# Kernel optimization log

Measured on AMD Instinct MI355X. Metric: run time of the kernel, lower is better.

Reference implementation:

```python
import jax, jax.numpy as jnp
import numpy as np
from jax import lax

T = 16        # in_length
E = 32        # input_embedding_size_d
H = 64        # encoder_size
NG = 32       # vehicles per scene group
G = 1024      # number of scene groups
N = G * NG    # total vehicles
C = 3         # class_num

leaky = lambda x: jax.nn.leaky_relu(x, 0.1)

def _gru_final(x_seq, Wih, Whh, bih, bhh):
    # x_seq: (T, N, E). PyTorch GRU gate order: r, z, n. Returns final hidden (N, H).
    def step(h, x):
        gx = x @ Wih.T + bih
        gh = h @ Whh.T + bhh
        xr, xz, xn = jnp.split(gx, 3, axis=-1)
        hr, hz, hn = jnp.split(gh, 3, axis=-1)
        r = jax.nn.sigmoid(xr + hr)
        z = jax.nn.sigmoid(xz + hz)
        ng = jnp.tanh(xn + r * hn)
        return (1.0 - z) * ng + z * h, None
    h0 = jnp.zeros((x_seq.shape[1], Whh.shape[1]), x_seq.dtype)
    hT, _ = lax.scan(step, h0, x_seq)
    return hT

def setup_inputs() -> dict:
    key = jax.random.key(0)
    ks = jax.random.split(key, 24)
    def rn(k, shape, fan):
        return jax.random.normal(k, shape, jnp.float32) * np.float32(1.0 / np.sqrt(fan))
    inp = {}
    inp["scene"] = jax.random.normal(ks[0], (N, 2 * T), jnp.float32)
    inp["condition"] = jax.random.randint(ks[1], (N,), 0, C, jnp.int32)
    inp["hero_pos_index"] = jax.random.randint(ks[2], (G,), 0, N, jnp.int32)
    inp["nbrs_pos_index"] = jax.random.randint(ks[3], (N,), 0, N, jnp.int32)
    inp["index_div"] = jnp.arange(N, dtype=jnp.int32).reshape(G, NG)
    # ip_emb_d: Linear(2, E)
    inp["W_emb"] = rn(ks[4], (2, E), 2)
    inp["b_emb"] = jnp.zeros((E,), jnp.float32)
    # forward / backward GRUs (weight_ih: (3H,E), weight_hh: (3H,H))
    inp["Wih_f"] = rn(ks[5], (3 * H, E), E); inp["Whh_f"] = rn(ks[6], (3 * H, H), H)
    inp["bih_f"] = jnp.zeros((3 * H,), jnp.float32); inp["bhh_f"] = jnp.zeros((3 * H,), jnp.float32)
    inp["Wih_b"] = rn(ks[7], (3 * H, E), E); inp["Whh_b"] = rn(ks[8], (3 * H, H), H)
    inp["bih_b"] = jnp.zeros((3 * H,), jnp.float32); inp["bhh_b"] = jnp.zeros((3 * H,), jnp.float32)
    # mlp: Linear(H, H//2)
    inp["Wm"] = rn(ks[9], (H, H // 2), H); inp["bm"] = jnp.zeros((H // 2,), jnp.float32)
    # spatial_mlp: Linear(2T, H) -> Linear(H, H//2)
    inp["Ws1"] = rn(ks[10], (2 * T, H), 2 * T); inp["bs1"] = jnp.zeros((H,), jnp.float32)
    inp["Ws2"] = rn(ks[11], (H, H // 2), H); inp["bs2"] = jnp.zeros((H // 2,), jnp.float32)
    # op_d: Linear(H, H//4) -> Linear(H//4, C)
    inp["Wo1"] = rn(ks[12], (H, H // 4), H); inp["bo1"] = jnp.zeros((H // 4,), jnp.float32)
    inp["Wo2"] = rn(ks[13], (H // 4, C), H // 4); inp["bo2"] = jnp.zeros((C,), jnp.float32)
    return inp

def reference(scene, condition, hero_pos_index, nbrs_pos_index, index_div,
              W_emb, b_emb, Wih_f, Whh_f, bih_f, bhh_f, Wih_b, Whh_b, bih_b, bhh_b,
              Wm, bm, Ws1, bs1, Ws2, bs2, Wo1, bo1, Wo2, bo2):
    n_total = scene.shape[0]
    # scene.view(-1,2,T).permute(2,0,1) -> (T, N, 2)
    scene_t = scene.reshape(n_total, 2, T).transpose(2, 0, 1)
    emb = leaky(scene_t @ W_emb + b_emb)                 # (T, N, E)
    h_f = _gru_final(emb, Wih_f, Whh_f, bih_f, bhh_f)    # (N, H)
    h_b = _gru_final(emb[::-1], Wih_b, Whh_b, bih_b, bhh_b)
    seq_enc = leaky(((h_f + h_b) * 0.5) @ Wm + bm)       # (N, H//2)
    # pairwise relative features within each group: rel[g, j, i] = x_i - x_j
    feat_g = scene[index_div]                            # (G, n, 2T); row layout == permute(1,2,0).view(-1,2T)
    rel = feat_g[:, None, :, :] - feat_g[:, :, None, :]  # (G, n, n, 2T)
    enc = leaky(leaky(rel @ Ws1 + bs1) @ Ws2 + bs2)      # (G, n, n, H//2)
    # diagonal pairs (i==j) are dropped in the original; subtract mlp(0) then divide by n-1
    zero_enc = leaky(leaky(bs1) @ Ws2 + bs2)             # (H//2,)
    n_grp = index_div.shape[1]
    pooled = (enc.sum(axis=2) - zero_enc) / (n_grp - 1)  # (G, n, H//2)
    pooled = pooled.reshape(n_total, -1)                 # group-concat order == vehicle order (arange groups)
    full_enc = jnp.concatenate([seq_enc, pooled], axis=1)  # (N, H)
    x_logit = leaky(full_enc @ Wo1 + bo1) @ Wo2 + bo2      # (N, C)
    return x_logit, full_enc
```

## Files before the change

### kernel.cpp

```cpp
#include <hip/hip_runtime.h>
#include <hip/hip_bf16.h>

#define TT 16
#define EE 32
#define HH 64
#define NGRP 32
#define CC 3

typedef __attribute__((ext_vector_type(8))) short short8;
typedef __attribute__((ext_vector_type(4))) short short4v;
typedef __attribute__((ext_vector_type(4))) float floatx4;

#define MFMA16(a, b, c) __builtin_amdgcn_mfma_f32_16x16x32_bf16((a), (b), (c), 0, 0, 0)

#define RLN2 1.4426950408889634f

__device__ __forceinline__ float leakyf(float x) { return fmaxf(x, 0.1f * x); }
__device__ __forceinline__ short f2bf(float x) {
    unsigned u = __float_as_uint(x);
    return (short)((u + 0x7FFFu + ((u >> 16) & 1u)) >> 16);
}
__device__ __forceinline__ short f2bf_h(float x) {
    return (short)((__float_as_uint(x) + 0x8000u) >> 16);
}
__device__ __forceinline__ float bf2f(short s) {
    return __uint_as_float(((unsigned)(unsigned short)s) << 16);
}
__device__ __forceinline__ short8 ld8bf(const float* __restrict__ p) {
    const float4 a = *(const float4*)p;
    const float4 b = *(const float4*)(p + 4);
    short8 v;
    v[0] = f2bf(a.x); v[1] = f2bf(a.y); v[2] = f2bf(a.z); v[3] = f2bf(a.w);
    v[4] = f2bf(b.x); v[5] = f2bf(b.y); v[6] = f2bf(b.z); v[7] = f2bf(b.w);
    return v;
}
__device__ __forceinline__ short8 ld8bfs(const float* __restrict__ p, float s) {
    const float4 a = *(const float4*)p;
    const float4 b = *(const float4*)(p + 4);
    short8 v;
    v[0] = f2bf(a.x * s); v[1] = f2bf(a.y * s); v[2] = f2bf(a.z * s); v[3] = f2bf(a.w * s);
    v[4] = f2bf(b.x * s); v[5] = f2bf(b.y * s); v[6] = f2bf(b.z * s); v[7] = f2bf(b.w * s);
    return v;
}

__global__ __launch_bounds__(512, 4) void fused_kernel(
    const float* __restrict__ scene, const int* __restrict__ index_div,
    const float* __restrict__ W_emb, const float* __restrict__ b_emb,
    const float* __restrict__ Wih_f, const float* __restrict__ Whh_f,
    const float* __restrict__ bih_f, const float* __restrict__ bhh_f,
    const float* __restrict__ Wih_b, const float* __restrict__ Whh_b,
    const float* __restrict__ bih_b, const float* __restrict__ bhh_b,
    const float* __restrict__ Wm, const float* __restrict__ bm,
    const float* __restrict__ Ws1, const float* __restrict__ bs1,
    const float* __restrict__ Ws2, const float* __restrict__ bs2,
    const float* __restrict__ Wo1, const float* __restrict__ bo1,
    const float* __restrict__ Wo2, const float* __restrict__ bo2,
    float* __restrict__ full_enc, float* __restrict__ out)
{
    __shared__ float sscene[32][33];
    __shared__ __align__(16) union SmemU {
        struct {
            short Hf[2 * 2 * 2 * 2 * 64 * 8];
            short Xb[2 * 2 * 2 * 64 * 8];
        } g;
        struct {
            short Hf_keep[2 * 2 * 2 * 2 * 64 * 8];
            float su[NGRP][68];
            float fe[NGRP][68];
            float szero[32];
        } s;
    } sm;

    const int g    = blockIdx.x;
    const int tid  = threadIdx.x;
    const int lane = tid & 63;
    const int w    = __builtin_amdgcn_readfirstlane(tid >> 6);
    const int dir  = w >> 2;
    const int wd   = w & 3;
    const int cc   = lane & 15;
    const int quad = lane >> 4;
    const int j    = wd * 16 + cc;
    const int ks_w = j >> 5;
    const int qa_w = (j >> 3) & 3;
    const int ii_w = j & 7;
    const int rlane = (lane & 48) | ((lane & 3) << 2) | ((lane >> 2) & 3);

    #pragma unroll
    for (int rep = 0; rep < 2; ++rep) {
        const int idx = tid + rep * 512;
        const int v = idx >> 5, c = idx & 31;
        const int n = index_div[g * NGRP + v];
        sscene[c][v] = scene[n * 32 + c];
    }

    const float* Wih = dir ? Wih_b : Wih_f;
    const float* Whh = dir ? Whh_b : Whh_f;
    const float* bih = dir ? bih_b : bih_f;
    const float* bhh = dir ? bhh_b : bhh_f;
    const int k0 = quad * 8;
    const float SRZ = -RLN2, SN = 2.0f * RLN2;
    const short8 Br0  = ld8bfs(Whh + (j      ) * 64 + k0,      SRZ);
    const short8 Br1  = ld8bfs(Whh + (j      ) * 64 + 32 + k0, SRZ);
    const short8 Br2  = ld8bfs(Wih + (j      ) * 32 + k0,      SRZ);
    const short8 Bz0  = ld8bfs(Whh + (j +  64) * 64 + k0,      SRZ);
    const short8 Bz1  = ld8bfs(Whh + (j +  64) * 64 + 32 + k0, SRZ);
    const short8 Bz2  = ld8bfs(Wih + (j +  64) * 32 + k0,      SRZ);
    const short8 Bhn0 = ld8bfs(Whh + (j + 128) * 64 + k0,      SN);
    const short8 Bhn1 = ld8bfs(Whh + (j + 128) * 64 + 32 + k0, SN);
    const short8 Bxn  = ld8bfs(Wih + (j + 128) * 32 + k0,      SN);
    const float vb_r  = SRZ * (bih[j] + bhh[j]);
    const float vb_z  = SRZ * (bih[j + 64] + bhh[j + 64]);
    const float vb_xn = SN * bih[j + 128];
    const float vb_hn = SN * bhh[j + 128];

    const int l     = tid & 255;
    const int veh_x = l & 31;
    const int q2    = l >> 5;
    const int e0    = q2 * 4;
    float w0e[4], w1e[4], bbe[4];
    #pragma unroll
    for (int d = 0; d < 4; ++d) {
        w0e[d] = W_emb[e0 + d];
        w1e[d] = W_emb[EE + e0 + d];
        bbe[d] = b_emb[e0 + d];
    }
    const int xoff = dir * 2048 + ((veh_x >> 4) * 64 + (q2 >> 1) * 16 + (veh_x & 15)) * 8
                   + (q2 & 1) * 4;

    __syncthreads();

    {
        const short8 z8 = {0, 0, 0, 0, 0, 0, 0, 0};
        *(short8*)&sm.g.Hf[(tid >> 8) * 4096 + (tid & 255) * 8] = z8;
        const int t0 = dir ? (TT - 1) : 0;
        const float xs = sscene[t0][veh_x];
        const float ys = sscene[16 + t0][veh_x];
        short4v v;
        #pragma unroll
        for (int d = 0; d < 4; ++d)
            v[d] = f2bf_h(leakyf(fmaf(xs, w0e[d], fmaf(ys, w1e[d], bbe[d]))));
        *(short4v*)&sm.g.Xb[xoff] = v;
    }

    float h_reg[8];
    #pragma unroll
    for (int i = 0; i < 8; ++i) h_reg[i] = 0.0f;

    const int hf_dir = dir * 4096;
    __syncthreads();

    #pragma unroll 2
    for (int s = 0; s < TT; ++s) {
        const int pb = s & 1, nb = pb ^ 1;
        const short* HfD = &sm.g.Hf[hf_dir + pb * 2048];
        short*       HfN = &sm.g.Hf[hf_dir + nb * 2048];
        const short* XbD = &sm.g.Xb[dir * 2048 + pb * 1024];
        #pragma unroll
        for (int mt = 0; mt < 2; ++mt) {
            const short8 Ah0 = *(const short8*)&HfD[((0 * 2 + mt) * 64 + rlane) * 8];
            const short8 Ah1 = *(const short8*)&HfD[((1 * 2 + mt) * 64 + rlane) * 8];
            const short8 Axx = *(const short8*)&XbD[(mt * 64 + lane) * 8];
            const floatx4 z4 = {0.f, 0.f, 0.f, 0.f};
            const floatx4 ar  = MFMA16(Axx, Br2, MFMA16(Ah1, Br1, MFMA16(Ah0, Br0, z4)));
            const floatx4 az  = MFMA16(Axx, Bz2, MFMA16(Ah1, Bz1, MFMA16(Ah0, Bz0, z4)));
            const floatx4 ahn = MFMA16(Ah1, Bhn1, MFMA16(Ah0, Bhn0, z4));
            const floatx4 axn = MFMA16(Axx, Bxn, z4);
            #pragma unroll
            for (int r = 0; r < 4; ++r) {
                const float rr = __builtin_amdgcn_rcpf(1.0f + __builtin_amdgcn_exp2f(ar[r] + vb_r));
                const float zz = __builtin_amdgcn_rcpf(1.0f + __builtin_amdgcn_exp2f(az[r] + vb_z));
                const float y  = fmaf(rr, ahn[r] + vb_hn, axn[r] + vb_xn);
                const float ng = fmaf(-2.0f,
                                      __builtin_amdgcn_rcpf(__builtin_amdgcn_exp2f(y) + 1.0f),
                                      1.0f);
                const float h0 = h_reg[mt * 4 + r];
                h_reg[mt * 4 + r] = fmaf(zz, h0 - ng, ng);
            }
        }
        #pragma unroll
        for (int mt = 0; mt < 2; ++mt) {
            #pragma unroll
            for (int r = 0; r < 4; ++r) {
                const int slot = qa_w * 16 + r * 4 + quad;
                HfN[((ks_w * 2 + mt) * 64 + slot) * 8 + ii_w] = f2bf_h(h_reg[mt * 4 + r]);
            }
        }
        if (s + 1 < TT) {
            const int tn = dir ? (TT - 2 - s) : (s + 1);
            const float xs = sscene[tn][veh_x];
            const float ys = sscene[16 + tn][veh_x];
            short4v v;
            #pragma unroll
            for (int d = 0; d < 4; ++d)
                v[d] = f2bf_h(leakyf(fmaf(xs, w0e[d], fmaf(ys, w1e[d], bbe[d]))));
            *(short4v*)&sm.g.Xb[xoff + nb * 1024] = v;
        }
        __syncthreads();
    }

    if (w < 4) {
        const int nt   = w >> 1;
        const int mt_e = w & 1;
        const int n_col = nt * 16 + cc;
        short8 Bm0, Bm1;
        #pragma unroll
        for (int i = 0; i < 8; ++i) {
            Bm0[i] = f2bf(Wm[(     quad * 8 + i) * 32 + n_col]);
            Bm1[i] = f2bf(Wm[(32 + quad * 8 + i) * 32 + n_col]);
        }
        short8 A0, A1;
        #pragma unroll
        for (int ks = 0; ks < 2; ++ks) {
            const short8 F = *(const short8*)&sm.g.Hf[0    + ((ks * 2 + mt_e) * 64 + rlane) * 8];
            const short8 B = *(const short8*)&sm.g.Hf[4096 + ((ks * 2 + mt_e) * 64 + rlane) * 8];
            #pragma unroll
            for (int i = 0; i < 8; ++i) {
                const short v = f2bf(0.5f * (bf2f(F[i]) + bf2f(B[i])));
                if (ks == 0) A0[i] = v; else A1[i] = v;
            }
        }
        const floatx4 z4 = {0.f, 0.f, 0.f, 0.f};
        const floatx4 acc = MFMA16(A1, Bm1, MFMA16(A0, Bm0, z4));
        const float bmn = bm[n_col];
        #pragma unroll
        for (int r = 0; r < 4; ++r) {
            const int veh = mt_e * 16 + quad * 4 + r;
            const float sv = leakyf(acc[r] + bmn);
            const int n = index_div[g * NGRP + veh];
            full_enc[n * HH + n_col] = sv;
            sm.s.fe[veh][n_col] = sv;
        }
    } else {
        const int v  = l >> 3;
        const int d0 = (l & 7) * 8;
        float acc[8];
        #pragma unroll
        for (int i = 0; i < 8; ++i) acc[i] = 0.0f;
        #pragma unroll
        for (int e = 0; e < EE; ++e) {
            const float f = sscene[e][v];
            const float4 w0 = *(const float4*)&Ws1[e * 64 + d0];
            const float4 w1 = *(const float4*)&Ws1[e * 64 + d0 + 4];
            acc[0] = fmaf(f, w0.x, acc[0]); acc[1] = fmaf(f, w0.y, acc[1]);
            acc[2] = fmaf(f, w0.z, acc[2]); acc[3] = fmaf(f, w0.w, acc[3]);
            acc[4] = fmaf(f, w1.x, acc[4]); acc[5] = fmaf(f, w1.y, acc[5]);
            acc[6] = fmaf(f, w1.z, acc[6]); acc[7] = fmaf(f, w1.w, acc[7]);
        }
        #pragma unroll
        for (int i = 0; i < 8; ++i) sm.s.su[v][d0 + i] = acc[i];
        if (l < 32) {
            float zs = bs2[l];
            #pragma unroll
            for (int d = 0; d < HH; ++d) zs = fmaf(leakyf(bs1[d]), Ws2[d * 32 + l], zs);
            sm.s.szero[l] = leakyf(zs);
        }
    }

    short8 Bw00, Bw01, Bw10, Bw11;
    #pragma unroll
    for (int i = 0; i < 8; ++i) {
        Bw00[i] = f2bf(Ws2[(     quad * 8 + i) * 32 + cc]);
        Bw01[i] = f2bf(Ws2[(32 + quad * 8 + i) * 32 + cc]);
        Bw10[i] = f2bf(Ws2[(     quad * 8 + i) * 32 + 16 + cc]);
        Bw11[i] = f2bf(Ws2[(32 + quad * 8 + i) * 32 + 16 + cc]);
    }
    float bsq0[8], bsq1[8];
    #pragma unroll
    for (int i = 0; i < 8; ++i) {
        bsq0[i] = bs1[quad * 8 + i];
        bsq1[i] = bs1[32 + quad * 8 + i];
    }
    const float bs2c0 = bs2[cc], bs2c1 = bs2[16 + cc];
    __syncthreads();

    float* swo1 = (float*)&sscene[0][0];
    *(float2*)&swo1[tid * 2] = *(const float2*)&Wo1[tid * 2];

    #pragma unroll 2
    for (int jj = 0; jj < 4; ++jj) {
        const int jrow = w * 4 + jj;
        float vj0[8], vj1[8];
        #pragma unroll
        for (int i = 0; i < 8; ++i) {
            vj0[i] = sm.s.su[jrow][quad * 8 + i] - bsq0[i];
            vj1[i] = sm.s.su[jrow][32 + quad * 8 + i] - bsq1[i];
        }
        float acc0 = 0.0f, acc1 = 0.0f;
        #pragma unroll
        for (int it = 0; it < 2; ++it) {
            const int irow = it * 16 + cc;
            const float4 p0 = *(const float4*)&sm.s.su[irow][quad * 8];
            const float4 p1 = *(const float4*)&sm.s.su[irow][quad * 8 + 4];
            const float4 p2 = *(const float4*)&sm.s.su[irow][32 + quad * 8];
            const float4 p3 = *(const float4*)&sm.s.su[irow][32 + quad * 8 + 4];
            short8 A0, A1;
            A0[0] = f2bf(leakyf(p0.x - vj0[0])); A0[1] = f2bf(leakyf(p0.y - vj0[1]));
            A0[2] = f2bf(leakyf(p0.z - vj0[2])); A0[3] = f2bf(leakyf(p0.w - vj0[3]));
            A0[4] = f2bf(leakyf(p1.x - vj0[4])); A0[5] = f2bf(leakyf(p1.y - vj0[5]));
            A0[6] = f2bf(leakyf(p1.z - vj0[6])); A0[7] = f2bf(leakyf(p1.w - vj0[7]));
            A1[0] = f2bf(leakyf(p2.x - vj1[0])); A1[1] = f2bf(leakyf(p2.y - vj1[1]));
            A1[2] = f2bf(leakyf(p2.z - vj1[2])); A1[3] = f2bf(leakyf(p2.w - vj1[3]));
            A1[4] = f2bf(leakyf(p3.x - vj1[4])); A1[5] = f2bf(leakyf(p3.y - vj1[5]));
            A1[6] = f2bf(leakyf(p3.z - vj1[6])); A1[7] = f2bf(leakyf(p3.w - vj1[7]));
            const floatx4 z4 = {0.f, 0.f, 0.f, 0.f};
            const floatx4 D0 = MFMA16(A1, Bw01, MFMA16(A0, Bw00, z4));
            const floatx4 D1 = MFMA16(A1, Bw11, MFMA16(A0, Bw10, z4));
            #pragma unroll
            for (int r = 0; r < 4; ++r) {
                acc0 += leakyf(D0[r] + bs2c0);
                acc1 += leakyf(D1[r] + bs2c1);
            }
        }
        acc0 += __shfl_xor(acc0, 16, 64); acc0 += __shfl_xor(acc0, 32, 64);
        acc1 += __shfl_xor(acc1, 16, 64); acc1 += __shfl_xor(acc1, 32, 64);
        const int n = index_div[g * NGRP + jrow];
        if (quad == 0) {
            const float pv = (acc0 - sm.s.szero[cc]) * (1.0f / 31.0f);
            full_enc[n * HH + 32 + cc] = pv;
            sm.s.fe[jrow][32 + cc] = pv;
        } else if (quad == 1) {
            const float pv = (acc1 - sm.s.szero[16 + cc]) * (1.0f / 31.0f);
            full_enc[n * HH + 48 + cc] = pv;
            sm.s.fe[jrow][48 + cc] = pv;
        }
    }
    __syncthreads();

    {
        const int veh = tid >> 4;
        const int p   = tid & 15;
        float a = bo1[p];
        #pragma unroll
        for (int k = 0; k < HH; ++k)
            a = fmaf(sm.s.fe[veh][k], swo1[k * 16 + p], a);
        a = leakyf(a);
        float l0 = a * Wo2[p * 3 + 0];
        float l1 = a * Wo2[p * 3 + 1];
        float l2 = a * Wo2[p * 3 + 2];
        #pragma unroll
        for (int off = 1; off < 16; off <<= 1) {
            l0 += __shfl_xor(l0, off, 64);
            l1 += __shfl_xor(l1, off, 64);
            l2 += __shfl_xor(l2, off, 64);
        }
        if (p == 0) {
            const int n = index_div[g * NGRP + veh];
            out[n * 3 + 0] = l0 + bo2[0];
            out[n * 3 + 1] = l1 + bo2[1];
            out[n * 3 + 2] = l2 + bo2[2];
        }
    }
}

extern "C" void kernel_launch(void* const* d_in, const int* in_sizes, int n_in,
                              void* d_out, int out_size, void* d_ws, size_t ws_size,
                              hipStream_t stream) {
    const float* scene     = (const float*)d_in[0];
    const int*   index_div = (const int*)d_in[4];
    const float* W_emb = (const float*)d_in[5];
    const float* b_emb = (const float*)d_in[6];
    const float* Wih_f = (const float*)d_in[7];
    const float* Whh_f = (const float*)d_in[8];
    const float* bih_f = (const float*)d_in[9];
    const float* bhh_f = (const float*)d_in[10];
    const float* Wih_b = (const float*)d_in[11];
    const float* Whh_b = (const float*)d_in[12];
    const float* bih_b = (const float*)d_in[13];
    const float* bhh_b = (const float*)d_in[14];
    const float* Wm  = (const float*)d_in[15];
    const float* bm  = (const float*)d_in[16];
    const float* Ws1 = (const float*)d_in[17];
    const float* bs1 = (const float*)d_in[18];
    const float* Ws2 = (const float*)d_in[19];
    const float* bs2 = (const float*)d_in[20];
    const float* Wo1 = (const float*)d_in[21];
    const float* bo1 = (const float*)d_in[22];
    const float* Wo2 = (const float*)d_in[23];
    const float* bo2 = (const float*)d_in[24];

    const int N = in_sizes[0] / (2 * TT);
    const int G = in_sizes[4] / NGRP;

    float* out      = (float*)d_out;
    float* full_enc = out + (size_t)N * CC;

    fused_kernel<<<dim3(G), dim3(512), 0, stream>>>(
        scene, index_div, W_emb, b_emb, Wih_f, Whh_f, bih_f, bhh_f,
        Wih_b, Whh_b, bih_b, bhh_b, Wm, bm, Ws1, bs1, Ws2, bs2,
        Wo1, bo1, Wo2, bo2, full_enc, out);
}
```

Before: 195.4 us.

## Split fused kernel into per-direction GRU kernel and separate tail kernel

The single 512-thread fused kernel, which ran both GRU directions and then the pooling and output heads, is split in two. A GRU kernel launches one 256-thread block per (group, direction) and writes the final hidden states as bf16 to workspace. A tail kernel then does the seq MLP, the pairwise spatial pooling and the output head per group. The aim is more independent blocks and less LDS per block, so the serial recurrence gets better occupancy and latency hiding and no longer shares a barrier with the other direction. The cost is an extra launch and a global-memory round trip for the hidden states. The hidden-state LDS layout is also changed to drop the rlane permutation.

```diff
diff --git a/kernel.cpp b/kernel.cpp
--- a/kernel.cpp
+++ b/kernel.cpp
@@ -43,51 +43,35 @@
     return v;
 }
 
-__global__ __launch_bounds__(512, 4) void fused_kernel(
+__global__ __launch_bounds__(256, 6) void gru_dir_kernel(
     const float* __restrict__ scene, const int* __restrict__ index_div,
     const float* __restrict__ W_emb, const float* __restrict__ b_emb,
     const float* __restrict__ Wih_f, const float* __restrict__ Whh_f,
     const float* __restrict__ bih_f, const float* __restrict__ bhh_f,
     const float* __restrict__ Wih_b, const float* __restrict__ Whh_b,
     const float* __restrict__ bih_b, const float* __restrict__ bhh_b,
-    const float* __restrict__ Wm, const float* __restrict__ bm,
-    const float* __restrict__ Ws1, const float* __restrict__ bs1,
-    const float* __restrict__ Ws2, const float* __restrict__ bs2,
-    const float* __restrict__ Wo1, const float* __restrict__ bo1,
-    const float* __restrict__ Wo2, const float* __restrict__ bo2,
-    float* __restrict__ full_enc, float* __restrict__ out)
+    short* __restrict__ hws)
 {
     __shared__ float sscene[32][33];
-    __shared__ __align__(16) union SmemU {
-        struct {
-            short Hf[2 * 2 * 2 * 2 * 64 * 8];
-            short Xb[2 * 2 * 2 * 64 * 8];
-        } g;
-        struct {
-            short Hf_keep[2 * 2 * 2 * 2 * 64 * 8];
-            float su[NGRP][68];
-            float fe[NGRP][68];
-            float szero[32];
-        } s;
-    } sm;
-
-    const int g    = blockIdx.x;
+    __shared__ __align__(16) short Hf[2 * 2 * 2 * 64 * 8];
+    __shared__ __align__(16) short Xb[2 * 2 * 64 * 8];
+
+    const int bx   = blockIdx.x;
+    const int g    = bx >> 1;
+    const int dir  = bx & 1;
     const int tid  = threadIdx.x;
     const int lane = tid & 63;
-    const int w    = __builtin_amdgcn_readfirstlane(tid >> 6);
-    const int dir  = w >> 2;
-    const int wd   = w & 3;
+    const int wd   = __builtin_amdgcn_readfirstlane(tid >> 6);
     const int cc   = lane & 15;
     const int quad = lane >> 4;
     const int j    = wd * 16 + cc;
     const int ks_w = j >> 5;
     const int qa_w = (j >> 3) & 3;
     const int ii_w = j & 7;
-    const int rlane = (lane & 48) | ((lane & 3) << 2) | ((lane >> 2) & 3);
-
-    #pragma unroll
-    for (int rep = 0; rep < 2; ++rep) {
-        const int idx = tid + rep * 512;
+
+    #pragma unroll
+    for (int rep = 0; rep < 4; ++rep) {
+        const int idx = tid + rep * 256;
         const int v = idx >> 5, c = idx & 31;
         const int n = index_div[g * NGRP + v];
         sscene[c][v] = scene[n * 32 + c];
@@ -113,9 +97,8 @@
     const float vb_xn = SN * bih[j + 128];
     const float vb_hn = SN * bhh[j + 128];
 
-    const int l     = tid & 255;
-    const int veh_x = l & 31;
-    const int q2    = l >> 5;
+    const int veh_x = tid & 31;
+    const int q2    = tid >> 5;
     const int e0    = q2 * 4;
     float w0e[4], w1e[4], bbe[4];
     #pragma unroll
@@ -124,14 +107,14 @@
         w1e[d] = W_emb[EE + e0 + d];
         bbe[d] = b_emb[e0 + d];
     }
-    const int xoff = dir * 2048 + ((veh_x >> 4) * 64 + (q2 >> 1) * 16 + (veh_x & 15)) * 8
+    const int xoff = ((veh_x >> 4) * 64 + (q2 >> 1) * 16 + (veh_x & 15)) * 8
                    + (q2 & 1) * 4;
 
     __syncthreads();
 
     {
         const short8 z8 = {0, 0, 0, 0, 0, 0, 0, 0};
-        *(short8*)&sm.g.Hf[(tid >> 8) * 4096 + (tid & 255) * 8] = z8;
+        *(short8*)&Hf[tid * 8] = z8;
         const int t0 = dir ? (TT - 1) : 0;
         const float xs = sscene[t0][veh_x];
         const float ys = sscene[16 + t0][veh_x];
@@ -139,26 +122,25 @@
         #pragma unroll
         for (int d = 0; d < 4; ++d)
             v[d] = f2bf_h(leakyf(fmaf(xs, w0e[d], fmaf(ys, w1e[d], bbe[d]))));
-        *(short4v*)&sm.g.Xb[xoff] = v;
+        *(short4v*)&Xb[xoff] = v;
     }
 
     float h_reg[8];
     #pragma unroll
     for (int i = 0; i < 8; ++i) h_reg[i] = 0.0f;
 
-    const int hf_dir = dir * 4096;
     __syncthreads();
 
     #pragma unroll 2
     for (int s = 0; s < TT; ++s) {
         const int pb = s & 1, nb = pb ^ 1;
-        const short* HfD = &sm.g.Hf[hf_dir + pb * 2048];
-        short*       HfN = &sm.g.Hf[hf_dir + nb * 2048];
-        const short* XbD = &sm.g.Xb[dir * 2048 + pb * 1024];
+        const short* HfD = &Hf[pb * 2048];
+        short*       HfN = &Hf[nb * 2048];
+        const short* XbD = &Xb[pb * 1024];
         #pragma unroll
         for (int mt = 0; mt < 2; ++mt) {
-            const short8 Ah0 = *(const short8*)&HfD[((0 * 2 + mt) * 64 + rlane) * 8];
-            const short8 Ah1 = *(const short8*)&HfD[((1 * 2 + mt) * 64 + rlane) * 8];
+            const short8 Ah0 = *(const short8*)&HfD[((0 * 2 + mt) * 64 + lane) * 8];
+            const short8 Ah1 = *(const short8*)&HfD[((1 * 2 + mt) * 64 + lane) * 8];
             const short8 Axx = *(const short8*)&XbD[(mt * 64 + lane) * 8];
             const floatx4 z4 = {0.f, 0.f, 0.f, 0.f};
             const floatx4 ar  = MFMA16(Axx, Br2, MFMA16(Ah1, Br1, MFMA16(Ah0, Br0, z4)));
@@ -181,7 +163,7 @@
         for (int mt = 0; mt < 2; ++mt) {
             #pragma unroll
             for (int r = 0; r < 4; ++r) {
-                const int slot = qa_w * 16 + r * 4 + quad;
+                const int slot = qa_w * 16 + quad * 4 + r;
                 HfN[((ks_w * 2 + mt) * 64 + slot) * 8 + ii_w] = f2bf_h(h_reg[mt * 4 + r]);
             }
         }
@@ -193,46 +175,55 @@
             #pragma unroll
             for (int d = 0; d < 4; ++d)
                 v[d] = f2bf_h(leakyf(fmaf(xs, w0e[d], fmaf(ys, w1e[d], bbe[d]))));
-            *(short4v*)&sm.g.Xb[xoff + nb * 1024] = v;
+            *(short4v*)&Xb[xoff + nb * 1024] = v;
         }
         __syncthreads();
     }
-
-    if (w < 4) {
-        const int nt   = w >> 1;
-        const int mt_e = w & 1;
-        const int n_col = nt * 16 + cc;
-        short8 Bm0, Bm1;
-        #pragma unroll
-        for (int i = 0; i < 8; ++i) {
-            Bm0[i] = f2bf(Wm[(     quad * 8 + i) * 32 + n_col]);
-            Bm1[i] = f2bf(Wm[(32 + quad * 8 + i) * 32 + n_col]);
-        }
-        short8 A0, A1;
-        #pragma unroll
-        for (int ks = 0; ks < 2; ++ks) {
-            const short8 F = *(const short8*)&sm.g.Hf[0    + ((ks * 2 + mt_e) * 64 + rlane) * 8];
-            const short8 B = *(const short8*)&sm.g.Hf[4096 + ((ks * 2 + mt_e) * 64 + rlane) * 8];
-            #pragma unroll
-            for (int i = 0; i < 8; ++i) {
-                const short v = f2bf(0.5f * (bf2f(F[i]) + bf2f(B[i])));
-                if (ks == 0) A0[i] = v; else A1[i] = v;
-            }
-        }
-        const floatx4 z4 = {0.f, 0.f, 0.f, 0.f};
-        const floatx4 acc = MFMA16(A1, Bm1, MFMA16(A0, Bm0, z4));
-        const float bmn = bm[n_col];
-        #pragma unroll
-        for (int r = 0; r < 4; ++r) {
-            const int veh = mt_e * 16 + quad * 4 + r;
-            const float sv = leakyf(acc[r] + bmn);
-            const int n = index_div[g * NGRP + veh];
-            full_enc[n * HH + n_col] = sv;
-            sm.s.fe[veh][n_col] = sv;
-        }
-    } else {
-        const int v  = l >> 3;
-        const int d0 = (l & 7) * 8;
+    *(short8*)&hws[(size_t)bx * 2048 + tid * 8] = *(const short8*)&Hf[tid * 8];
+}
+
+__global__ __launch_bounds__(256, 4) void tail_kernel(
+    const float* __restrict__ scene, const int* __restrict__ index_div,
+    const short* __restrict__ hws,
+    const float* __restrict__ Wm, const float* __restrict__ bm,
+    const float* __restrict__ Ws1, const float* __restrict__ bs1,
+    const float* __restrict__ Ws2, const float* __restrict__ bs2,
+    const float* __restrict__ Wo1, const float* __restrict__ bo1,
+    const float* __restrict__ Wo2, const float* __restrict__ bo2,
+    float* __restrict__ full_enc, float* __restrict__ out)
+{
+    __shared__ float sscene[32][33];
+    __shared__ float su[NGRP][68];
+    __shared__ float fe[NGRP][68];
+    __shared__ float swo1[1024];
+    __shared__ float szero[32];
+
+    const int g    = blockIdx.x;
+    const int tid  = threadIdx.x;
+    const int lane = tid & 63;
+    const int w    = __builtin_amdgcn_readfirstlane(tid >> 6);
+    const int cc   = lane & 15;
+    const int quad = lane >> 4;
+
+    #pragma unroll
+    for (int rep = 0; rep < 4; ++rep) {
+        const int idx = tid + rep * 256;
+        const int v = idx >> 5, c = idx & 31;
+        const int n = index_div[g * NGRP + v];
+        sscene[c][v] = scene[n * 32 + c];
+    }
+    *(float4*)&swo1[tid * 4] = *(const float4*)&Wo1[tid * 4];
+    if (tid < 32) {
+        float zs = bs2[tid];
+        #pragma unroll
+        for (int d = 0; d < HH; ++d) zs = fmaf(leakyf(bs1[d]), Ws2[d * 32 + tid], zs);
+        szero[tid] = leakyf(zs);
+    }
+    __syncthreads();
+
+    {
+        const int v  = tid >> 3;
+        const int d0 = (tid & 7) * 8;
         float acc[8];
         #pragma unroll
         for (int i = 0; i < 8; ++i) acc[i] = 0.0f;
@@ -247,12 +238,40 @@
             acc[6] = fmaf(f, w1.z, acc[6]); acc[7] = fmaf(f, w1.w, acc[7]);
         }
         #pragma unroll
-        for (int i = 0; i < 8; ++i) sm.s.su[v][d0 + i] = acc[i];
-        if (l < 32) {
-            float zs = bs2[l];
+        for (int i = 0; i < 8; ++i) su[v][d0 + i] = acc[i];
+    }
+
+    {
+        const int nt   = w >> 1;
+        const int mt_e = w & 1;
+        const int n_col = nt * 16 + cc;
+        short8 Bm0, Bm1;
+        #pragma unroll
+        for (int i = 0; i < 8; ++i) {
+            Bm0[i] = f2bf(Wm[(     quad * 8 + i) * 32 + n_col]);
+            Bm1[i] = f2bf(Wm[(32 + quad * 8 + i) * 32 + n_col]);
+        }
+        short8 A0, A1;
+        #pragma unroll
+        for (int ks = 0; ks < 2; ++ks) {
+            const short8 F = *(const short8*)&hws[(size_t)(g * 2 + 0) * 2048 + ((ks * 2 + mt_e) * 64 + lane) * 8];
+            const short8 B = *(const short8*)&hws[(size_t)(g * 2 + 1) * 2048 + ((ks * 2 + mt_e) * 64 + lane) * 8];
             #pragma unroll
-            for (int d = 0; d < HH; ++d) zs = fmaf(leakyf(bs1[d]), Ws2[d * 32 + l], zs);
-            sm.s.szero[l] = leakyf(zs);
+            for (int i = 0; i < 8; ++i) {
+                const short v = f2bf(0.5f * (bf2f(F[i]) + bf2f(B[i])));
+                if (ks == 0) A0[i] = v; else A1[i] = v;
+            }
+        }
+        const floatx4 z4 = {0.f, 0.f, 0.f, 0.f};
+        const floatx4 acc = MFMA16(A1, Bm1, MFMA16(A0, Bm0, z4));
+        const float bmn = bm[n_col];
+        #pragma unroll
+        for (int r = 0; r < 4; ++r) {
+            const int veh = mt_e * 16 + quad * 4 + r;
+            const float sv = leakyf(acc[r] + bmn);
+            const int n = index_div[g * NGRP + veh];
+            full_enc[n * HH + n_col] = sv;
+            fe[veh][n_col] = sv;
         }
     }
 
@@ -273,26 +292,23 @@
     const float bs2c0 = bs2[cc], bs2c1 = bs2[16 + cc];
     __syncthreads();
 
-    float* swo1 = (float*)&sscene[0][0];
-    *(float2*)&swo1[tid * 2] = *(const float2*)&Wo1[tid * 2];
-
     #pragma unroll 2
-    for (int jj = 0; jj < 4; ++jj) {
-        const int jrow = w * 4 + jj;
+    for (int jj = 0; jj < 8; ++jj) {
+        const int jrow = w * 8 + jj;
         float vj0[8], vj1[8];
         #pragma unroll
         for (int i = 0; i < 8; ++i) {
-            vj0[i] = sm.s.su[jrow][quad * 8 + i] - bsq0[i];
-            vj1[i] = sm.s.su[jrow][32 + quad * 8 + i] - bsq1[i];
+            vj0[i] = su[jrow][quad * 8 + i] - bsq0[i];
+            vj1[i] = su[jrow][32 + quad * 8 + i] - bsq1[i];
         }
         float acc0 = 0.0f, acc1 = 0.0f;
         #pragma unroll
         for (int it = 0; it < 2; ++it) {
             const int irow = it * 16 + cc;
-            const float4 p0 = *(const float4*)&sm.s.su[irow][quad * 8];
-            const float4 p1 = *(const float4*)&sm.s.su[irow][quad * 8 + 4];
-            const float4 p2 = *(const float4*)&sm.s.su[irow][32 + quad * 8];
-            const float4 p3 = *(const float4*)&sm.s.su[irow][32 + quad * 8 + 4];
+            const float4 p0 = *(const float4*)&su[irow][quad * 8];
+            const float4 p1 = *(const float4*)&su[irow][quad * 8 + 4];
+            const float4 p2 = *(const float4*)&su[irow][32 + quad * 8];
+            const float4 p3 = *(const float4*)&su[irow][32 + quad * 8 + 4];
             short8 A0, A1;
             A0[0] = f2bf(leakyf(p0.x - vj0[0])); A0[1] = f2bf(leakyf(p0.y - vj0[1]));
             A0[2] = f2bf(leakyf(p0.z - vj0[2])); A0[3] = f2bf(leakyf(p0.w - vj0[3]));
@@ -315,30 +331,35 @@
         acc1 += __shfl_xor(acc1, 16, 64); acc1 += __shfl_xor(acc1, 32, 64);
         const int n = index_div[g * NGRP + jrow];
         if (quad == 0) {
-            const float pv = (acc0 - sm.s.szero[cc]) * (1.0f / 31.0f);
+            const float pv = (acc0 - szero[cc]) * (1.0f / 31.0f);
             full_enc[n * HH + 32 + cc] = pv;
-            sm.s.fe[jrow][32 + cc] = pv;
+            fe[jrow][32 + cc] = pv;
         } else if (quad == 1) {
-            const float pv = (acc1 - sm.s.szero[16 + cc]) * (1.0f / 31.0f);
+            const float pv = (acc1 - szero[16 + cc]) * (1.0f / 31.0f);
             full_enc[n * HH + 48 + cc] = pv;
-            sm.s.fe[jrow][48 + cc] = pv;
+            fe[jrow][48 + cc] = pv;
         }
     }
     __syncthreads();
 
     {
-        const int veh = tid >> 4;
-        const int p   = tid & 15;
-        float a = bo1[p];
-        #pragma unroll
-        for (int k = 0; k < HH; ++k)
-            a = fmaf(sm.s.fe[veh][k], swo1[k * 16 + p], a);
-        a = leakyf(a);
-        float l0 = a * Wo2[p * 3 + 0];
-        float l1 = a * Wo2[p * 3 + 1];
-        float l2 = a * Wo2[p * 3 + 2];
-        #pragma unroll
-        for (int off = 1; off < 16; off <<= 1) {
+        const int veh = tid >> 3;
+        const int p   = tid & 7;
+        const int m0  = p * 2;
+        float a0 = bo1[m0], a1 = bo1[m0 + 1];
+        #pragma unroll
+        for (int k = 0; k < HH; ++k) {
+            const float f = fe[veh][k];
+            const float2 wv = *(const float2*)&swo1[k * 16 + m0];
+            a0 = fmaf(f, wv.x, a0);
+            a1 = fmaf(f, wv.y, a1);
+        }
+        a0 = leakyf(a0); a1 = leakyf(a1);
+        float l0 = fmaf(a0, Wo2[m0 * 3 + 0], a1 * Wo2[(m0 + 1) * 3 + 0]);
+        float l1 = fmaf(a0, Wo2[m0 * 3 + 1], a1 * Wo2[(m0 + 1) * 3 + 1]);
+        float l2 = fmaf(a0, Wo2[m0 * 3 + 2], a1 * Wo2[(m0 + 1) * 3 + 2]);
+        #pragma unroll
+        for (int off = 1; off < 8; off <<= 1) {
             l0 += __shfl_xor(l0, off, 64);
             l1 += __shfl_xor(l1, off, 64);
             l2 += __shfl_xor(l2, off, 64);
@@ -383,9 +404,13 @@
 
     float* out      = (float*)d_out;
     float* full_enc = out + (size_t)N * CC;
-
-    fused_kernel<<<dim3(G), dim3(512), 0, stream>>>(
+    short* hws      = (short*)d_ws;
+
+    gru_dir_kernel<<<dim3(2 * G), dim3(256), 0, stream>>>(
         scene, index_div, W_emb, b_emb, Wih_f, Whh_f, bih_f, bhh_f,
-        Wih_b, Whh_b, bih_b, bhh_b, Wm, bm, Ws1, bs1, Ws2, bs2,
+        Wih_b, Whh_b, bih_b, bhh_b, hws);
+
+    tail_kernel<<<dim3(G), dim3(256), 0, stream>>>(
+        scene, index_div, hws, Wm, bm, Ws1, bs1, Ws2, bs2,
         Wo1, bo1, Wo2, bo2, full_enc, out);
 }
```

Result: slower. 274.0 us (+40.2%).
